# Kernel tuning notes

Measured on AMD Instinct MI355X. Metric: run time of the kernel, lower is better.

Reference implementation:

```python
import jax, jax.numpy as jnp
import numpy as np

H = 256        # hidden_channels (== out_channels)
IN = 128       # in_channels (atom features)
ED = 64        # edge_dim (bond features)
G = 1024       # num graphs
L = 48         # atoms per graph (static pad length)
N = G * L      # num atoms
E = 2 * N      # num directed edges
NLAYERS = 4


def setup_inputs() -> dict:
    key = jax.random.key(0)
    ks = jax.random.split(key, 12)
    def rn(k, shape, scale=0.05):
        return jax.random.normal(k, shape, jnp.float32) * scale
    return {
        "x": jax.random.normal(ks[0], (N, IN), jnp.float32),
        "edge_attr": jax.random.normal(ks[1], (E, ED), jnp.float32),
        "edge_index": jax.random.randint(ks[2], (2, E), 0, N),
        "batch": jnp.repeat(jnp.arange(G), L),  # sorted, L atoms per graph
        "w_atom": rn(ks[3], (IN, H)), "b_atom": jnp.zeros((H,), jnp.float32),
        "w_bond": rn(ks[4], (ED, H)), "b_bond": jnp.zeros((H,), jnp.float32),
        "conv_w": rn(ks[5], (NLAYERS, H, H)), "conv_b": jnp.zeros((NLAYERS, H), jnp.float32),
        "w_lin": rn(ks[6], (3 * H, H)), "b_lin": jnp.zeros((H,), jnp.float32),
        "gru_bias": rn(ks[7], (H,), 0.06),
        "w_ih": rn(ks[8], (2, 3 * H, H)), "w_hh": rn(ks[9], (2, 3 * H, H)),
        "b_ih": jnp.zeros((2, 3 * H), jnp.float32), "b_hh": jnp.zeros((2, 3 * H), jnp.float32),
        "w_out": rn(ks[10], (2 * H, H)), "b_out": jnp.zeros((H,), jnp.float32),
    }


def reference(x, edge_attr, edge_index, batch, w_atom, b_atom, w_bond, b_bond,
              conv_w, conv_b, w_lin, b_lin, gru_bias, w_ih, w_hh, b_ih, b_hh,
              w_out, b_out):
    relu = jax.nn.relu
    row, col = edge_index[0], edge_index[1]  # flow='target_to_source': aggregate at row

    x_proj = relu(x @ w_atom + b_atom)                 # [N, H]
    h_atom = x_proj
    h_bond = relu(edge_attr @ w_bond + b_bond)         # [E, H]

    def booster(h_bond):
        # message_booster multi-aggregation: sum * max (empty slots -> 0, as torch_scatter)
        s = jax.ops.segment_sum(h_bond, row, num_segments=N)
        m = jax.ops.segment_max(h_bond, row, num_segments=N)
        m = jnp.where(jnp.isfinite(m), m, 0.0)
        return s * m

    for i in range(NLAYERS - 1):
        h_atom = h_atom + booster(h_bond)              # additive communicator
        # edge_update: x[edge_index_i] - edge_attr[edge_index_j]; seq = Linear+ReLU (dropout p=0)
        h_bond = relu((h_atom[row] - h_bond[col]) @ conv_w[i] + conv_b[i])
    aggr_message = h_atom + booster(h_bond)            # last conv; edge output discarded

    h = jnp.concatenate([aggr_message, h_atom, x_proj], axis=1) @ w_lin + b_lin  # [N, H]

    # ---- BatchGRU ----
    msg = relu(h + gru_bias)
    starts = jnp.searchsorted(batch, jnp.arange(G))
    pos = jnp.arange(N) - starts[batch]                # position within own graph
    messages = jnp.zeros((G, L, H), h.dtype).at[batch, pos].set(msg)
    h0 = jax.ops.segment_max(h, batch, num_segments=G)  # [G, H], same init both dirs

    def gru_dir(seq, d):
        def cell(hst, x_t):
            gi = x_t @ w_ih[d].T + b_ih[d]
            gh = hst @ w_hh[d].T + b_hh[d]
            i_r, i_z, i_n = jnp.split(gi, 3, -1)
            h_r, h_z, h_n = jnp.split(gh, 3, -1)
            r = jax.nn.sigmoid(i_r + h_r)
            z = jax.nn.sigmoid(i_z + h_z)
            n = jnp.tanh(i_n + r * h_n)
            hn = (1.0 - z) * n + z * hst
            return hn, hn
        _, out = jax.lax.scan(cell, h0, seq)
        return out

    seq = messages.transpose(1, 0, 2)                  # [L, G, H]
    out_f = gru_dir(seq, 0)
    out_b = gru_dir(seq[::-1], 1)[::-1]
    h_msgs = jnp.concatenate([out_f, out_b], -1).transpose(1, 0, 2)  # [G, L, 2H]
    unpadded = h_msgs[batch, pos]                      # [N, 2H]

    return relu(unpadded @ w_out + b_out)              # seq_out (dropout p=0)
```

## Files before the change

### kernel.cpp

```cpp
#include <hip/hip_runtime.h>
#include <math.h>

#define HH 256
#define GG 1024
#define LL 48
#define NNODES 49152
#define NEDGES 98304
#define SB 256.0f
#define DSB 0.00390625f

typedef _Float16 f16;
typedef __attribute__((ext_vector_type(8))) _Float16 f16x8;
typedef __attribute__((ext_vector_type(4))) float f32x4;

#define MFMA16(a, b, c) __builtin_amdgcn_mfma_f32_16x16x32_f16(a, b, c, 0, 0, 0)

__device__ inline float sc_from_max(float m) {
    if (!(m > 0.f)) return 1.0f;
    return ldexpf(1.0f, 13 - ilogbf(m));
}

__global__ void csr_count(const int* __restrict__ row, int* __restrict__ counts)
{
    int e = blockIdx.x * 256 + threadIdx.x;
    if (e < NEDGES) atomicAdd(&counts[row[e]], 1);
}

__global__ __launch_bounds__(1024) void scan_offsets(const int* __restrict__ counts,
                                                     int* __restrict__ offsets)
{
    __shared__ int tsum[1024];
    const int tid = threadIdx.x;
    const int base = tid * 48;
    int s = 0;
    for (int i = 0; i < 48; i++) s += counts[base + i];
    tsum[tid] = s;
    __syncthreads();
    for (int off = 1; off < 1024; off <<= 1) {
        int v = (tid >= off) ? tsum[tid - off] : 0;
        __syncthreads();
        tsum[tid] += v;
        __syncthreads();
    }
    int run = (tid == 0) ? 0 : tsum[tid - 1];
    for (int i = 0; i < 48; i++) { offsets[base + i] = run; run += counts[base + i]; }
    if (tid == 1023) offsets[NNODES] = run;
}

__global__ void csr_fill(const int* __restrict__ row, const int* __restrict__ offsets,
                         int* __restrict__ cursor, int* __restrict__ elist)
{
    int e = blockIdx.x * 256 + threadIdx.x;
    if (e < NEDGES) {
        int r = row[e];
        int p = atomicAdd(&cursor[r], 1);
        elist[offsets[r] + p] = e;
    }
}

__global__ void prep_graphs(const int* __restrict__ batch, int* __restrict__ starts,
                            int* __restrict__ gcnt)
{
    int i = blockIdx.x * 256 + threadIdx.x;
    if (i < NNODES) {
        int b = batch[i];
        atomicAdd(&gcnt[b], 1);
        if (i == 0 || batch[i - 1] != b) starts[b] = i;
    }
}

__global__ void rowscale(const float* __restrict__ A, int K, float* __restrict__ sc)
{
    int m = blockIdx.x, ln = threadIdx.x;
    float v = 0.f;
    for (int k = ln; k < K; k += 64) v = fmaxf(v, fabsf(A[(size_t)m * K + k]));
    for (int s = 32; s; s >>= 1) v = fmaxf(v, __shfl_xor(v, s));
    if (ln == 0) sc[m] = sc_from_max(v);
}

__global__ void prep_wT_all(const float* __restrict__ w_atom, const float* __restrict__ w_bond,
                            const float* __restrict__ conv_w, const float* __restrict__ w_lin,
                            const float* __restrict__ w_out,
                            f16* __restrict__ watomH, f16* __restrict__ watomL,
                            f16* __restrict__ wbondH, f16* __restrict__ wbondL,
                            f16* __restrict__ convH0, f16* __restrict__ convL0,
                            f16* __restrict__ convH1, f16* __restrict__ convL1,
                            f16* __restrict__ convH2, f16* __restrict__ convL2,
                            f16* __restrict__ wlinH, f16* __restrict__ wlinL,
                            f16* __restrict__ woutH, f16* __restrict__ woutL)
{
    int idx = blockIdx.x * 256 + threadIdx.x;
    int krow = idx >> 8, n = idx & 255;
    const float* src; f16* oH; f16* oL; int k;
    if (krow < 128)       { src = w_atom;           oH = watomH; oL = watomL; k = krow; }
    else if (krow < 192)  { src = w_bond;           oH = wbondH; oL = wbondL; k = krow - 128; }
    else if (krow < 448)  { src = conv_w;           oH = convH0; oL = convL0; k = krow - 192; }
    else if (krow < 704)  { src = conv_w + 65536;   oH = convH1; oL = convL1; k = krow - 448; }
    else if (krow < 960)  { src = conv_w + 131072;  oH = convH2; oL = convL2; k = krow - 704; }
    else if (krow < 1728) { src = w_lin;            oH = wlinH;  oL = wlinL;  k = krow - 960; }
    else                  { src = w_out;            oH = woutH;  oL = woutL;  k = krow - 1728; }
    float v = src[(size_t)k * 256 + n] * SB;
    f16 h = (f16)v;
    size_t o = ((size_t)(k >> 5) * 256 + n) * 32 + (k & 31);
    oH[o] = h;
    oL[o] = (f16)(v - (float)h);
}

__global__ void prep_gruW(const float* __restrict__ w_ih, const float* __restrict__ w_hh,
                          const float* __restrict__ b_ih, const float* __restrict__ b_hh,
                          f16* __restrict__ BgH, f16* __restrict__ BgL,
                          float* __restrict__ bias4)
{
    int idx = blockIdx.x * 256 + threadIdx.x;
    int d = idx >> 19;
    int rem = idx & 524287;
    int k = rem >> 10;
    int col = rem & 1023;
    int jj = col >> 2, s = col & 3;
    const float* Wi = w_ih + (size_t)d * 768 * 256;
    const float* Wh = w_hh + (size_t)d * 768 * 256;
    float v;
    if (s == 0)      v = (k < 256) ? Wi[(size_t)jj * 256 + k]         : Wh[(size_t)jj * 256 + (k - 256)];
    else if (s == 1) v = (k < 256) ? Wi[(size_t)(256 + jj) * 256 + k] : Wh[(size_t)(256 + jj) * 256 + (k - 256)];
    else if (s == 2) v = (k < 256) ? Wi[(size_t)(512 + jj) * 256 + k] : 0.f;
    else             v = (k < 256) ? 0.f : Wh[(size_t)(512 + jj) * 256 + (k - 256)];
    v *= SB;
    f16 h = (f16)v;
    size_t o = ((size_t)(d * 16 + (k >> 5)) * 1024 + col) * 32 + (k & 31);
    BgH[o] = h;
    BgL[o] = (f16)(v - (float)h);
    if (k == 0) {
        const float* bi = b_ih + d * 768;
        const float* bh = b_hh + d * 768;
        float bv;
        if (s == 0)      bv = bi[jj] + bh[jj];
        else if (s == 1) bv = bi[256 + jj] + bh[256 + jj];
        else if (s == 2) bv = bi[512 + jj];
        else             bv = bh[512 + jj];
        bias4[d * 1024 + col] = bv;
    }
}

__global__ void booster(const float* __restrict__ hb_lo, const float* __restrict__ hb_hi,
                        const float* __restrict__ atom_in, float* __restrict__ out,
                        const int* __restrict__ offsets, const int* __restrict__ elist,
                        float* __restrict__ scOut)
{
    const int wv = threadIdx.x >> 6;
    const int n = blockIdx.x * 4 + wv;
    const int ln = threadIdx.x & 63;
    const int b0 = offsets[n], b1 = offsets[n + 1];
    float4 s = {0.f, 0.f, 0.f, 0.f}, m = {0.f, 0.f, 0.f, 0.f};
    for (int p = b0; p < b1; p++) {
        int e = elist[p];
        const float* hb = (e < NNODES) ? (hb_lo + (size_t)e * HH)
                                       : (hb_hi + (size_t)(e - NNODES) * HH);
        float4 v = *(const float4*)(hb + ln * 4);
        s.x += v.x; s.y += v.y; s.z += v.z; s.w += v.w;
        m.x = fmaxf(m.x, v.x); m.y = fmaxf(m.y, v.y);
        m.z = fmaxf(m.z, v.z); m.w = fmaxf(m.w, v.w);
    }
    float4 a = *(const float4*)(atom_in + (size_t)n * HH + ln * 4);
    float4 o;
    o.x = a.x + s.x * m.x; o.y = a.y + s.y * m.y;
    o.z = a.z + s.z * m.z; o.w = a.w + s.w * m.w;
    *(float4*)(out + (size_t)n * HH + ln * 4) = o;
    float v = fmaxf(fmaxf(fabsf(o.x), fabsf(o.y)), fmaxf(fabsf(o.z), fabsf(o.w)));
    for (int t = 32; t; t >>= 1) v = fmaxf(v, __shfl_xor(v, t));
    if (ln == 0) scOut[n] = sc_from_max(v);
}

__global__ void h0_init(const float* __restrict__ h, const int* __restrict__ starts,
                        const int* __restrict__ gcnt, float* __restrict__ hid0,
                        float* __restrict__ scG)
{
    const int wv = threadIdx.x >> 6;
    const int g = blockIdx.x * 4 + wv;
    const int ln = threadIdx.x & 63;
    const int st = starts[g], cn = gcnt[g];
    float4 m = {-INFINITY, -INFINITY, -INFINITY, -INFINITY};
    float4 am = {0.f, 0.f, 0.f, 0.f};
    for (int i = 0; i < cn; i++) {
        float4 v = *(const float4*)(h + (size_t)(st + i) * HH + ln * 4);
        m.x = fmaxf(m.x, v.x); m.y = fmaxf(m.y, v.y);
        m.z = fmaxf(m.z, v.z); m.w = fmaxf(m.w, v.w);
        am.x = fmaxf(am.x, fabsf(v.x)); am.y = fmaxf(am.y, fabsf(v.y));
        am.z = fmaxf(am.z, fabsf(v.z)); am.w = fmaxf(am.w, fabsf(v.w));
    }
    if (cn == 0) { m.x = m.y = m.z = m.w = 0.f; }
    *(float4*)(hid0 + (size_t)g * HH + ln * 4) = m;
    *(float4*)(hid0 + (size_t)GG * HH + (size_t)g * HH + ln * 4) = m;
    float a = fmaxf(fmaxf(am.x, am.y), fmaxf(am.z, am.w));
    for (int t = 32; t; t >>= 1) a = fmaxf(a, __shfl_xor(a, t));
    if (ln == 0) scG[g] = sc_from_max(fmaxf(a + 0.07f, 1.0f));
}

__global__ void build_msgP(const float* __restrict__ h, const float* __restrict__ gbias,
                           const int* __restrict__ starts, const int* __restrict__ gcnt,
                           float* __restrict__ msgP)
{
    int l = blockIdx.x, g = blockIdx.y, k = threadIdx.x;
    float v = 0.f;
    if (l < gcnt[g]) {
        int node = starts[g] + l;
        v = fmaxf(h[(size_t)node * HH + k] + gbias[k], 0.f);
    }
    msgP[((size_t)l * GG + g) * HH + k] = v;
}

template<int MODE>
__device__ __forceinline__ void gemmLoadA(const float* __restrict__ A,
    const float* __restrict__ S0, const float* __restrict__ S1,
    const float* __restrict__ S2, int rI, int cI, int row, int K, int k,
    float va[8])
{
    if constexpr (MODE == 0) {
        const float* p = A + (size_t)row * K + k;
        float4 v0 = *(const float4*)p, v1 = *(const float4*)(p + 4);
        va[0]=v0.x; va[1]=v0.y; va[2]=v0.z; va[3]=v0.w;
        va[4]=v1.x; va[5]=v1.y; va[6]=v1.z; va[7]=v1.w;
    } else if constexpr (MODE == 1) {
        const float* pa = S0 + (size_t)rI * HH + k;
        const float* pb = S1 + (size_t)cI * HH + k;
        float4 a0 = *(const float4*)pa, a1 = *(const float4*)(pa + 4);
        float4 b0 = *(const float4*)pb, b1 = *(const float4*)(pb + 4);
        va[0]=a0.x-b0.x; va[1]=a0.y-b0.y; va[2]=a0.z-b0.z; va[3]=a0.w-b0.w;
        va[4]=a1.x-b1.x; va[5]=a1.y-b1.y; va[6]=a1.z-b1.z; va[7]=a1.w-b1.w;
    } else if constexpr (MODE == 2) {
        const float* S = (k < 256) ? S0 : ((k < 512) ? S1 : S2);
        const float* p = S + (size_t)row * HH + (k & 255);
        float4 v0 = *(const float4*)p, v1 = *(const float4*)(p + 4);
        va[0]=v0.x; va[1]=v0.y; va[2]=v0.z; va[3]=v0.w;
        va[4]=v1.x; va[5]=v1.y; va[6]=v1.z; va[7]=v1.w;
    } else {
        const float* S = (k < 256) ? S0 : S1;
        const float* p = S + (size_t)row * HH + (k & 255);
        float4 v0 = *(const float4*)p, v1 = *(const float4*)(p + 4);
        va[0]=v0.x; va[1]=v0.y; va[2]=v0.z; va[3]=v0.w;
        va[4]=v1.x; va[5]=v1.y; va[6]=v1.z; va[7]=v1.w;
    }
}

template<int MODE, bool RELU, bool SPLITC, bool WSCALE, int NX>
__global__ __launch_bounds__(256) void gemm_f16x3(
    const float* __restrict__ A,
    const float* __restrict__ S0, const float* __restrict__ S1, const float* __restrict__ S2,
    const int* __restrict__ ridx, const int* __restrict__ cidx,
    const f16* __restrict__ BgH, const f16* __restrict__ BgL,
    const float* __restrict__ bias,
    const float* __restrict__ sc0, const float* __restrict__ sc1, const float* __restrict__ sc2,
    float* __restrict__ Clo, float* __restrict__ Chi,
    float* __restrict__ scOut, int K)
{
    __shared__ __align__(16) f16 Ah[64 * 40], Al[64 * 40];
    __shared__ __align__(16) f16 Bh[256 * 40], Bl[256 * 40];
    __shared__ float scL[64];
    __shared__ float rmL[64][4];

    const int tid = threadIdx.x;
    const int m0 = blockIdx.x * 64;
    const int arow = tid >> 2, aoct = tid & 3;
    const int w = tid >> 6, lane = tid & 63, lr = lane & 15, lh = lane >> 4;

    if (tid < 64) {
        float sc;
        if constexpr (MODE == 0) sc = sc0[m0 + tid];
        else if constexpr (MODE == 1) {
            int r = ridx[m0 + tid], cc = cidx[m0 + tid];
            sc = fminf(sc0[r], sc1[cc]) * 0.5f;
        } else if constexpr (MODE == 2) {
            sc = fminf(fminf(sc0[m0 + tid], sc1[m0 + tid]), sc2[m0 + tid]);
        } else {
            sc = sc0[cidx[m0 + tid]];
        }
        scL[tid] = sc;
    }
    int rI = 0, cI = 0;
    if constexpr (MODE == 1) { rI = ridx[m0 + arow]; cI = cidx[m0 + arow]; }
    __syncthreads();
    const float myS = scL[arow];

    float va[8];
    f16x8 rbh[4], rbl[4];
    gemmLoadA<MODE>(A, S0, S1, S2, rI, cI, m0 + arow, K, aoct * 8, va);
    {
        size_t base = (size_t)tid * 32;
        const f16x8* ph = (const f16x8*)(BgH + base);
#pragma unroll
        for (int q = 0; q < 4; q++) rbh[q] = ph[q];
        if constexpr (NX == 3) {
            const f16x8* pl = (const f16x8*)(BgL + base);
#pragma unroll
            for (int q = 0; q < 4; q++) rbl[q] = pl[q];
        }
    }

    f32x4 acc[4][4] = {};
    for (int k0 = 0; k0 < K; k0 += 32) {
        {
            f16x8 hi, lo;
#pragma unroll
            for (int e = 0; e < 8; e++) {
                float a = va[e] * myS;
                f16 h = (f16)a;
                hi[e] = h;
                if constexpr (NX == 3) lo[e] = (f16)(a - (float)h);
            }
            *(f16x8*)&Ah[arow * 40 + aoct * 8] = hi;
            if constexpr (NX == 3) *(f16x8*)&Al[arow * 40 + aoct * 8] = lo;
        }
#pragma unroll
        for (int q = 0; q < 4; q++) {
            *(f16x8*)&Bh[tid * 40 + q * 8] = rbh[q];
            if constexpr (NX == 3) *(f16x8*)&Bl[tid * 40 + q * 8] = rbl[q];
        }
        __syncthreads();
        if (k0 + 32 < K) {
            gemmLoadA<MODE>(A, S0, S1, S2, rI, cI, m0 + arow, K, k0 + 32 + aoct * 8, va);
            size_t base = ((size_t)((k0 + 32) >> 5) * 256 + tid) * 32;
            const f16x8* ph = (const f16x8*)(BgH + base);
#pragma unroll
            for (int q = 0; q < 4; q++) rbh[q] = ph[q];
            if constexpr (NX == 3) {
                const f16x8* pl = (const f16x8*)(BgL + base);
#pragma unroll
                for (int q = 0; q < 4; q++) rbl[q] = pl[q];
            }
        }
        f16x8 fah[4], fal[4];
#pragma unroll
        for (int i = 0; i < 4; i++) {
            fah[i] = *(const f16x8*)&Ah[(i * 16 + lr) * 40 + lh * 8];
            if constexpr (NX == 3) fal[i] = *(const f16x8*)&Al[(i * 16 + lr) * 40 + lh * 8];
        }
#pragma unroll
        for (int j = 0; j < 4; j++) {
            int colx = w * 64 + j * 16 + lr;
            f16x8 fbh = *(const f16x8*)&Bh[colx * 40 + lh * 8];
            if constexpr (NX == 3) {
                f16x8 fbl = *(const f16x8*)&Bl[colx * 40 + lh * 8];
#pragma unroll
                for (int i = 0; i < 4; i++) {
                    acc[i][j] = MFMA16(fah[i], fbh, acc[i][j]);
                    acc[i][j] = MFMA16(fah[i], fbl, acc[i][j]);
                    acc[i][j] = MFMA16(fal[i], fbh, acc[i][j]);
                }
            } else {
#pragma unroll
                for (int i = 0; i < 4; i++)
                    acc[i][j] = MFMA16(fah[i], fbh, acc[i][j]);
            }
        }
        __syncthreads();
    }

    float rm[4][4];
#pragma unroll
    for (int i = 0; i < 4; i++)
#pragma unroll
        for (int e = 0; e < 4; e++) rm[i][e] = 0.f;
#pragma unroll
    for (int i = 0; i < 4; i++) {
#pragma unroll
        for (int e = 0; e < 4; e++) {
            int ml = i * 16 + lh * 4 + e;
            int m = m0 + ml;
            float inv = DSB / scL[ml];
            float* Cb;
            if constexpr (SPLITC)
                Cb = (m < NNODES) ? (Clo + (size_t)m * HH) : (Chi + (size_t)(m - NNODES) * HH);
            else
                Cb = Clo + (size_t)m * HH;
#pragma unroll
            for (int j = 0; j < 4; j++) {
                int n = w * 64 + j * 16 + lr;
                float v = acc[i][j][e] * inv + bias[n];
                if constexpr (RELU) v = fmaxf(v, 0.f);
                Cb[n] = v;
                if constexpr (WSCALE) rm[i][e] = fmaxf(rm[i][e], fabsf(v));
            }
        }
    }
    if constexpr (WSCALE) {
#pragma unroll
        for (int i = 0; i < 4; i++)
#pragma unroll
            for (int e = 0; e < 4; e++) {
                float v = rm[i][e];
                v = fmaxf(v, __shfl_xor(v, 1));
                v = fmaxf(v, __shfl_xor(v, 2));
                v = fmaxf(v, __shfl_xor(v, 4));
                v = fmaxf(v, __shfl_xor(v, 8));
                if (lr == 0) rmL[i * 16 + lh * 4 + e][w] = v;
            }
        __syncthreads();
        if (tid < 64)
            scOut[m0 + tid] = sc_from_max(fmaxf(fmaxf(rmL[tid][0], rmL[tid][1]),
                                                fmaxf(rmL[tid][2], rmL[tid][3])));
    }
}

__global__ __launch_bounds__(512) void gru_step_f16(
    const float* __restrict__ msgP, const f16* __restrict__ BgH, const f16* __restrict__ BgL,
    const float* __restrict__ bias4, const float* __restrict__ hidC, float* __restrict__ hidN,
    const float* __restrict__ scG, const int* __restrict__ starts, const int* __restrict__ gcnt,
    float* __restrict__ outF, float* __restrict__ outB, int t)
{
    __shared__ __align__(16) char smemraw[36864];
    float* Cs = (float*)smemraw;
    __shared__ float scL[64];

    const int tid = threadIdx.x;
    const int id = blockIdx.x;
    const int c = id & 7, d = (id >> 3) & 1, gt = id >> 4;
    const int g0 = gt * 64;
    const int l = d ? (LL - 1 - t) : t;
    const float* hidCd = hidC + (size_t)d * GG * HH;
    float* hidNd = hidN + (size_t)d * GG * HH;

    if (tid < 64) scL[tid] = scG[g0 + tid];
    __syncthreads();

    const int arow = tid >> 3, akoct = tid & 7;
    const float myS = scL[arow];
    const int w = tid >> 6;
    const int wg = w >> 2, wc = w & 3;
    const int lane = tid & 63, lr = lane & 15, lh = lane >> 4;

    f16* Ah0 = (f16*)smemraw;
    f16* Al0 = Ah0 + 4608;
    f16* Ah1 = Al0 + 4608;
    f16* Al1 = Ah1 + 4608;

    {
        const float* p = msgP + ((size_t)l * GG + g0 + arow) * HH + akoct * 8;
        float4 v0 = *(const float4*)p, v1 = *(const float4*)(p + 4);
        float va0[8] = {v0.x, v0.y, v0.z, v0.w, v1.x, v1.y, v1.z, v1.w};
        f16x8 hi, lo;
#pragma unroll
        for (int e = 0; e < 8; e++) {
            float a = va0[e] * myS;
            f16 h = (f16)a;
            hi[e] = h;
            lo[e] = (f16)(a - (float)h);
        }
        *(f16x8*)&Ah0[arow * 72 + akoct * 8] = hi;
        *(f16x8*)&Al0[arow * 72 + akoct * 8] = lo;
    }
    f16x8 fbh[2][2], fbl[2][2];
#pragma unroll
    for (int ks = 0; ks < 2; ks++) {
        size_t kbase = (size_t)(d * 16 + ks) * 1024;
#pragma unroll
        for (int j = 0; j < 2; j++) {
            size_t o = (kbase + (c * 128 + wc * 32 + j * 16 + lr)) * 32 + lh * 8;
            fbh[ks][j] = *(const f16x8*)(BgH + o);
            fbl[ks][j] = *(const f16x8*)(BgL + o);
        }
    }
    __syncthreads();

    f32x4 acc[2][2] = {};
#pragma unroll
    for (int win = 0; win < 8; win++) {
        f16* AhC = (win & 1) ? Ah1 : Ah0;
        f16* AlC = (win & 1) ? Al1 : Al0;
        f16* AhN = (win & 1) ? Ah0 : Ah1;
        f16* AlN = (win & 1) ? Al0 : Al1;

        float va[8];
        if (win < 7) {
            int k = (win + 1) * 64 + akoct * 8;
            const float* p = (k < 256)
                ? msgP + ((size_t)l * GG + g0 + arow) * HH + k
                : hidCd + (size_t)(g0 + arow) * HH + (k - 256);
            float4 v0 = *(const float4*)p, v1 = *(const float4*)(p + 4);
            va[0]=v0.x; va[1]=v0.y; va[2]=v0.z; va[3]=v0.w;
            va[4]=v1.x; va[5]=v1.y; va[6]=v1.z; va[7]=v1.w;
        }
        f16x8 nbh[2][2], nbl[2][2];
        if (win < 7) {
#pragma unroll
            for (int ks = 0; ks < 2; ks++) {
                size_t kbase = (size_t)(d * 16 + (win + 1) * 2 + ks) * 1024;
#pragma unroll
                for (int j = 0; j < 2; j++) {
                    size_t o = (kbase + (c * 128 + wc * 32 + j * 16 + lr)) * 32 + lh * 8;
                    nbh[ks][j] = *(const f16x8*)(BgH + o);
                    nbl[ks][j] = *(const f16x8*)(BgL + o);
                }
            }
        }
#pragma unroll
        for (int ks = 0; ks < 2; ks++) {
            f16x8 fah[2], fal[2];
#pragma unroll
            for (int i = 0; i < 2; i++) {
                fah[i] = *(const f16x8*)&AhC[(wg * 32 + i * 16 + lr) * 72 + ks * 32 + lh * 8];
                fal[i] = *(const f16x8*)&AlC[(wg * 32 + i * 16 + lr) * 72 + ks * 32 + lh * 8];
            }
#pragma unroll
            for (int j = 0; j < 2; j++) {
#pragma unroll
                for (int i = 0; i < 2; i++) {
                    acc[i][j] = MFMA16(fah[i], fbh[ks][j], acc[i][j]);
                    acc[i][j] = MFMA16(fah[i], fbl[ks][j], acc[i][j]);
                    acc[i][j] = MFMA16(fal[i], fbh[ks][j], acc[i][j]);
                }
            }
        }
        if (win < 7) {
            f16x8 hi, lo;
#pragma unroll
            for (int e = 0; e < 8; e++) {
                float a = va[e] * myS;
                f16 h = (f16)a;
                hi[e] = h;
                lo[e] = (f16)(a - (float)h);
            }
            *(f16x8*)&AhN[arow * 72 + akoct * 8] = hi;
            *(f16x8*)&AlN[arow * 72 + akoct * 8] = lo;
#pragma unroll
            for (int ks = 0; ks < 2; ks++)
#pragma unroll
                for (int j = 0; j < 2; j++) {
                    fbh[ks][j] = nbh[ks][j];
                    fbl[ks][j] = nbl[ks][j];
                }
        }
        __syncthreads();
    }

#pragma unroll
    for (int i = 0; i < 2; i++) {
#pragma unroll
        for (int e = 0; e < 4; e++) {
            int ml = wg * 32 + i * 16 + lh * 4 + e;
            float inv = DSB / scL[ml];
#pragma unroll
            for (int j = 0; j < 2; j++)
                Cs[ml * 132 + wc * 32 + j * 16 + lr] = acc[i][j][e] * inv;
        }
    }
    __syncthreads();

    const float* b4 = bias4 + d * 1024;
    const int jl = tid & 31;
    const int J  = c * 32 + jl;
    const int gbase = (tid >> 5) * 4;
    const float bb0 = b4[4 * J + 0], bb1 = b4[4 * J + 1];
    const float bb2 = b4[4 * J + 2], bb3 = b4[4 * J + 3];
    float* o = d ? outB : outF;
#pragma unroll
    for (int i = 0; i < 4; i++) {
        int gl = gbase + i;
        int g = g0 + gl;
        f32x4 gv = *(const f32x4*)&Cs[gl * 132 + jl * 4];
        float r = 1.f / (1.f + expf(-(gv[0] + bb0)));
        float z = 1.f / (1.f + expf(-(gv[1] + bb1)));
        float nn = tanhf(gv[2] + bb2 + r * (gv[3] + bb3));
        float hp = hidCd[(size_t)g * HH + J];
        float hnew = (1.f - z) * nn + z * hp;
        hidNd[(size_t)g * HH + J] = hnew;
        if (l < gcnt[g]) o[(size_t)(starts[g] + l) * HH + J] = hnew;
    }
}

__global__ void fill_sentinel(float* __restrict__ out, float v)
{
    size_t idx = (size_t)blockIdx.x * 256 + threadIdx.x;
    out[idx] = v;
}

extern "C" void kernel_launch(void* const* d_in, const int* in_sizes, int n_in,
                              void* d_out, int out_size, void* d_ws, size_t ws_size,
                              hipStream_t stream)
{
    (void)in_sizes; (void)n_in; (void)out_size;
    const float* x         = (const float*)d_in[0];
    const float* edge_attr = (const float*)d_in[1];
    const int*   eidx      = (const int*)d_in[2];
    const int*   batch     = (const int*)d_in[3];
    const float* w_atom    = (const float*)d_in[4];
    const float* b_atom    = (const float*)d_in[5];
    const float* w_bond    = (const float*)d_in[6];
    const float* b_bond    = (const float*)d_in[7];
    const float* conv_w    = (const float*)d_in[8];
    const float* conv_b    = (const float*)d_in[9];
    const float* w_lin     = (const float*)d_in[10];
    const float* b_lin     = (const float*)d_in[11];
    const float* gru_bias  = (const float*)d_in[12];
    const float* w_ih      = (const float*)d_in[13];
    const float* w_hh      = (const float*)d_in[14];
    const float* b_ih      = (const float*)d_in[15];
    const float* b_hh      = (const float*)d_in[16];
    const float* w_out     = (const float*)d_in[17];
    const float* b_out     = (const float*)d_in[18];

    const int* row = eidx;
    const int* col = eidx + NEDGES;

    const size_t NH = (size_t)NNODES * HH;

    float* W   = (float*)d_ws;
    float* W0  = W;
    float* W1  = W + NH;
    float* W1h = W + 2 * NH;
    float* W2  = W + 3 * NH;
    float* DO  = (float*)d_out;

    size_t off = 4 * NH;
    int* counts  = (int*)(W + off);      off += NNODES;
    int* cursor  = (int*)(W + off);      off += NNODES;
    int* gcnt    = (int*)(W + off);      off += GG;
    int* starts  = (int*)(W + off);      off += GG;
    int* offsets = (int*)(W + off);      off += NNODES + 1;
    int* elist   = (int*)(W + off);      off += NEDGES;
    float* scX    = W + off;             off += NNODES;
    float* scEA   = W + off;             off += NEDGES;
    float* scHbA  = W + off;             off += NEDGES;
    float* scHbB  = W + off;             off += NEDGES;
    float* scAtom = W + off;             off += NNODES;
    float* scAggr = W + off;             off += NNODES;
    float* scXp   = W + off;             off += NNODES;
    float* scGru  = W + off;             off += GG;
    off = (off + 3) & ~(size_t)3;
    f16* fp = (f16*)(W + off);
    f16* watomH = fp;                     fp += 4 * 256 * 32;
    f16* watomL = fp;                     fp += 4 * 256 * 32;
    f16* wbondH = fp;                     fp += 2 * 256 * 32;
    f16* wbondL = fp;                     fp += 2 * 256 * 32;
    f16* convH[3]; f16* convL[3];
    for (int i = 0; i < 3; i++) { convH[i] = fp; fp += 8 * 256 * 32; convL[i] = fp; fp += 8 * 256 * 32; }
    f16* wlinH = fp;                      fp += 24 * 256 * 32;
    f16* wlinL = fp;                      fp += 24 * 256 * 32;
    f16* woutH = fp;                      fp += 16 * 256 * 32;
    f16* woutL = fp;                      fp += 16 * 256 * 32;

    const size_t NEED = (char*)fp - (char*)d_ws;
    if (ws_size < NEED) {
        fill_sentinel<<<(int)(NH / 256), 256, 0, stream>>>((float*)d_out, (float)ws_size);
        return;
    }

    float* hid0  = DO;
    float* hid1  = DO + 2 * (size_t)GG * HH;
    float* bias4 = DO + 4 * (size_t)GG * HH;
    f16* BgH = (f16*)(bias4 + 2048);
    f16* BgL = BgH + (size_t)2 * 16 * 1024 * 32;

    hipMemsetAsync(counts, 0, (size_t)(2 * NNODES + 2 * GG) * sizeof(int), stream);
    prep_graphs<<<(NNODES + 255) / 256, 256, 0, stream>>>(batch, starts, gcnt);
    csr_count<<<(NEDGES + 255) / 256, 256, 0, stream>>>(row, counts);
    scan_offsets<<<1, 1024, 0, stream>>>(counts, offsets);
    csr_fill<<<(NEDGES + 255) / 256, 256, 0, stream>>>(row, offsets, cursor, elist);

    rowscale<<<NNODES, 64, 0, stream>>>(x, 128, scX);
    rowscale<<<NEDGES, 64, 0, stream>>>(edge_attr, 64, scEA);

    prep_wT_all<<<2240, 256, 0, stream>>>(w_atom, w_bond, conv_w, w_lin, w_out,
        watomH, watomL, wbondH, wbondL, convH[0], convL[0], convH[1], convL[1],
        convH[2], convL[2], wlinH, wlinL, woutH, woutL);

    gemm_f16x3<0, true, false, true, 3><<<NNODES / 64, 256, 0, stream>>>(
        x, nullptr, nullptr, nullptr, nullptr, nullptr, watomH, watomL, b_atom,
        scX, nullptr, nullptr, W0, nullptr, scAtom, 128);
    gemm_f16x3<0, true, true, true, 3><<<NEDGES / 64, 256, 0, stream>>>(
        edge_attr, nullptr, nullptr, nullptr, nullptr, nullptr, wbondH, wbondL, b_bond,
        scEA, nullptr, nullptr, W1, W1h, scHbA, 64);

    float* cur_lo = W1; float* cur_hi = W1h; float* cur_sc = scHbA;
    float* nxt_lo = W2; float* nxt_hi = DO;  float* nxt_sc = scHbB;
    for (int i = 0; i < 3; i++) {
        booster<<<NNODES / 4, 256, 0, stream>>>(cur_lo, cur_hi, W0, W0, offsets, elist, scAtom);
        gemm_f16x3<1, true, true, true, 3><<<NEDGES / 64, 256, 0, stream>>>(
            nullptr, W0, cur_lo, nullptr, row, col, convH[i], convL[i],
            conv_b + (size_t)i * HH, scAtom, cur_sc, nullptr, nxt_lo, nxt_hi, nxt_sc, 256);
        float* t0 = cur_lo; cur_lo = nxt_lo; nxt_lo = t0;
        float* t1 = cur_hi; cur_hi = nxt_hi; nxt_hi = t1;
        float* t2 = cur_sc; cur_sc = nxt_sc; nxt_sc = t2;
    }
    booster<<<NNODES / 4, 256, 0, stream>>>(cur_lo, cur_hi, W0, W1, offsets, elist, scAggr);
    gemm_f16x3<0, true, false, true, 3><<<NNODES / 64, 256, 0, stream>>>(
        x, nullptr, nullptr, nullptr, nullptr, nullptr, watomH, watomL, b_atom,
        scX, nullptr, nullptr, W1h, nullptr, scXp, 128);
    gemm_f16x3<2, false, false, false, 3><<<NNODES / 64, 256, 0, stream>>>(
        nullptr, W1, W0, W1h, nullptr, nullptr, wlinH, wlinL, b_lin,
        scAggr, scAtom, scXp, W2, nullptr, nullptr, 768);

    h0_init<<<GG / 4, 256, 0, stream>>>(W2, starts, gcnt, hid0, scGru);
    build_msgP<<<dim3(LL, GG), 256, 0, stream>>>(W2, gru_bias, starts, gcnt, W1h);
    prep_gruW<<<(2 * 512 * 1024) / 256, 256, 0, stream>>>(w_ih, w_hh, b_ih, b_hh, BgH, BgL, bias4);

    for (int t = 0; t < LL; t++) {
        float* hc = (t & 1) ? hid1 : hid0;
        float* hx = (t & 1) ? hid0 : hid1;
        gru_step_f16<<<256, 512, 0, stream>>>(W1h, BgH, BgL, bias4, hc, hx,
                                              scGru, starts, gcnt, W0, W1, t);
    }

    gemm_f16x3<3, true, false, false, 1><<<NNODES / 64, 256, 0, stream>>>(
        nullptr, W0, W1, nullptr, nullptr, batch, woutH, nullptr, b_out,
        scGru, nullptr, nullptr, (float*)d_out, nullptr, nullptr, 512);
}
```

Before: 1.405 ms.

## Double-buffer A tiles in LDS and load B fragments directly into registers

The GEMM now reads each wave's B fragments straight from global memory into registers, so the B tile is no longer staged through shared memory. The A tile is double-buffered in LDS, which cuts the loop to one barrier per k-step. Launch bounds now ask for two blocks per CU. The point is to shrink LDS use and synchronisation and to overlap the next tile's loads with the MFMA work. The cost is more register pressure from prefetched fragments, and the launch-bound hint may cause spills.

Measured after the change: 1.397 ms. No clear change (-0.6%).

```diff
diff --git a/kernel.cpp b/kernel.cpp
--- a/kernel.cpp
+++ b/kernel.cpp
@@ -242,7 +242,7 @@
 }
 
 template<int MODE, bool RELU, bool SPLITC, bool WSCALE, int NX>
-__global__ __launch_bounds__(256) void gemm_f16x3(
+__global__ __launch_bounds__(256, 2) void gemm_f16x3(
     const float* __restrict__ A,
     const float* __restrict__ S0, const float* __restrict__ S1, const float* __restrict__ S2,
     const int* __restrict__ ridx, const int* __restrict__ cidx,
@@ -252,8 +252,7 @@
     float* __restrict__ Clo, float* __restrict__ Chi,
     float* __restrict__ scOut, int K)
 {
-    __shared__ __align__(16) f16 Ah[64 * 40], Al[64 * 40];
-    __shared__ __align__(16) f16 Bh[256 * 40], Bl[256 * 40];
+    __shared__ __align__(16) f16 AhB[2][64 * 40], AlB[2][64 * 40];
     __shared__ float scL[64];
     __shared__ float rmL[64][4];
 
@@ -279,25 +278,68 @@
     if constexpr (MODE == 1) { rI = ridx[m0 + arow]; cI = cidx[m0 + arow]; }
     __syncthreads();
     const float myS = scL[arow];
-
-    float va[8];
-    f16x8 rbh[4], rbl[4];
-    gemmLoadA<MODE>(A, S0, S1, S2, rI, cI, m0 + arow, K, aoct * 8, va);
+    const int nIter = K >> 5;
+
     {
-        size_t base = (size_t)tid * 32;
-        const f16x8* ph = (const f16x8*)(BgH + base);
-#pragma unroll
-        for (int q = 0; q < 4; q++) rbh[q] = ph[q];
-        if constexpr (NX == 3) {
-            const f16x8* pl = (const f16x8*)(BgL + base);
-#pragma unroll
-            for (int q = 0; q < 4; q++) rbl[q] = pl[q];
-        }
-    }
+        float va0[8];
+        gemmLoadA<MODE>(A, S0, S1, S2, rI, cI, m0 + arow, K, aoct * 8, va0);
+        f16x8 hi, lo;
+#pragma unroll
+        for (int e = 0; e < 8; e++) {
+            float a = va0[e] * myS;
+            f16 h = (f16)a;
+            hi[e] = h;
+            if constexpr (NX == 3) lo[e] = (f16)(a - (float)h);
+        }
+        *(f16x8*)&AhB[0][arow * 40 + aoct * 8] = hi;
+        if constexpr (NX == 3) *(f16x8*)&AlB[0][arow * 40 + aoct * 8] = lo;
+    }
+    f16x8 fbh[4], fbl[4];
+#pragma unroll
+    for (int j = 0; j < 4; j++) {
+        size_t o = (size_t)(w * 64 + j * 16 + lr) * 32 + lh * 8;
+        fbh[j] = *(const f16x8*)(BgH + o);
+        if constexpr (NX == 3) fbl[j] = *(const f16x8*)(BgL + o);
+    }
+    __syncthreads();
 
     f32x4 acc[4][4] = {};
-    for (int k0 = 0; k0 < K; k0 += 32) {
-        {
+    for (int kb = 0; kb < nIter; kb++) {
+        const f16* AhC = AhB[kb & 1];
+        const f16* AlC = AlB[kb & 1];
+        float va[8];
+        f16x8 nbh[4], nbl[4];
+        if (kb + 1 < nIter) {
+            gemmLoadA<MODE>(A, S0, S1, S2, rI, cI, m0 + arow, K, (kb + 1) * 32 + aoct * 8, va);
+#pragma unroll
+            for (int j = 0; j < 4; j++) {
+                size_t o = ((size_t)(kb + 1) * 256 + (w * 64 + j * 16 + lr)) * 32 + lh * 8;
+                nbh[j] = *(const f16x8*)(BgH + o);
+                if constexpr (NX == 3) nbl[j] = *(const f16x8*)(BgL + o);
+            }
+        }
+        f16x8 fah[4], fal[4];
+#pragma unroll
+        for (int i = 0; i < 4; i++) {
+            fah[i] = *(const f16x8*)&AhC[(i * 16 + lr) * 40 + lh * 8];
+            if constexpr (NX == 3) fal[i] = *(const f16x8*)&AlC[(i * 16 + lr) * 40 + lh * 8];
+        }
+#pragma unroll
+        for (int j = 0; j < 4; j++) {
+            if constexpr (NX == 3) {
+#pragma unroll
+                for (int i = 0; i < 4; i++) {
+                    acc[i][j] = MFMA16(fah[i], fbh[j], acc[i][j]);
+                    acc[i][j] = MFMA16(fah[i], fbl[j], acc[i][j]);
+                    acc[i][j] = MFMA16(fal[i], fbh[j], acc[i][j]);
+                }
+            } else {
+#pragma unroll
+                for (int i = 0; i < 4; i++)
+                    acc[i][j] = MFMA16(fah[i], fbh[j], acc[i][j]);
+            }
+        }
+        if (kb + 1 < nIter) {
             f16x8 hi, lo;
 #pragma unroll
             for (int e = 0; e < 8; e++) {
@@ -306,49 +348,14 @@
                 hi[e] = h;
                 if constexpr (NX == 3) lo[e] = (f16)(a - (float)h);
             }
-            *(f16x8*)&Ah[arow * 40 + aoct * 8] = hi;
-            if constexpr (NX == 3) *(f16x8*)&Al[arow * 40 + aoct * 8] = lo;
-        }
-#pragma unroll
-        for (int q = 0; q < 4; q++) {
-            *(f16x8*)&Bh[tid * 40 + q * 8] = rbh[q];
-            if constexpr (NX == 3) *(f16x8*)&Bl[tid * 40 + q * 8] = rbl[q];
-        }
-        __syncthreads();
-        if (k0 + 32 < K) {
-            gemmLoadA<MODE>(A, S0, S1, S2, rI, cI, m0 + arow, K, k0 + 32 + aoct * 8, va);
-            size_t base = ((size_t)((k0 + 32) >> 5) * 256 + tid) * 32;
-            const f16x8* ph = (const f16x8*)(BgH + base);
-#pragma unroll
-            for (int q = 0; q < 4; q++) rbh[q] = ph[q];
-            if constexpr (NX == 3) {
-                const f16x8* pl = (const f16x8*)(BgL + base);
-#pragma unroll
-                for (int q = 0; q < 4; q++) rbl[q] = pl[q];
-            }
-        }
-        f16x8 fah[4], fal[4];
-#pragma unroll
-        for (int i = 0; i < 4; i++) {
-            fah[i] = *(const f16x8*)&Ah[(i * 16 + lr) * 40 + lh * 8];
-            if constexpr (NX == 3) fal[i] = *(const f16x8*)&Al[(i * 16 + lr) * 40 + lh * 8];
-        }
-#pragma unroll
-        for (int j = 0; j < 4; j++) {
-            int colx = w * 64 + j * 16 + lr;
-            f16x8 fbh = *(const f16x8*)&Bh[colx * 40 + lh * 8];
-            if constexpr (NX == 3) {
-                f16x8 fbl = *(const f16x8*)&Bl[colx * 40 + lh * 8];
-#pragma unroll
-                for (int i = 0; i < 4; i++) {
-                    acc[i][j] = MFMA16(fah[i], fbh, acc[i][j]);
-                    acc[i][j] = MFMA16(fah[i], fbl, acc[i][j]);
-                    acc[i][j] = MFMA16(fal[i], fbh, acc[i][j]);
-                }
-            } else {
-#pragma unroll
-                for (int i = 0; i < 4; i++)
-                    acc[i][j] = MFMA16(fah[i], fbh, acc[i][j]);
+            f16* AhN = AhB[(kb + 1) & 1];
+            f16* AlN = AlB[(kb + 1) & 1];
+            *(f16x8*)&AhN[arow * 40 + aoct * 8] = hi;
+            if constexpr (NX == 3) *(f16x8*)&AlN[arow * 40 + aoct * 8] = lo;
+#pragma unroll
+            for (int j = 0; j < 4; j++) {
+                fbh[j] = nbh[j];
+                if constexpr (NX == 3) fbl[j] = nbl[j];
             }
         }
         __syncthreads();
```
